# Kernel tuning notes

Measured on AMD Instinct MI355X. Metric: run time of the kernel, lower is better.

## Reference

```python
import jax, jax.numpy as jnp
import numpy as np

LOSS_WEIGHT = 1.0
EPS = 1e-08
OUT_H, OUT_W = 112, 96
NBINS = 256


def _nearest_resize(x, out_h, out_w):
    # torch F.interpolate default mode='nearest': src_idx = floor(dst_idx * in/out)
    B, C, H, W = x.shape
    hi = (jnp.arange(out_h) * H) // out_h
    wi = (jnp.arange(out_w) * W) // out_w
    return x[:, :, hi][:, :, :, wi]


def setup_inputs() -> dict:
    key = jax.random.key(0)
    k1, k2 = jax.random.split(key)
    x0 = jax.random.uniform(k1, (256, 3, 224, 192), dtype=jnp.float32) * 255.0
    img = jax.random.uniform(k2, (256, 3, OUT_H, OUT_W), dtype=jnp.float32) * 255.0
    return {"x0": x0, "img": img}


def reference(x0, img):
    # interpolate x0 to (112, 96), cast both to uint8 (truncation, values in [0,255])
    x0r = _nearest_resize(x0, OUT_H, OUT_W)
    ix = img.astype(jnp.uint8).astype(jnp.int32).ravel()   # x in hxx(img, x0)
    iy = x0r.astype(jnp.uint8).astype(jnp.int32).ravel()   # y

    # NOTE: faithful quirk — normalizer is last-dim size of img (=96), not n elements
    size = jnp.float32(img.shape[-1])

    hist_x = jnp.zeros(NBINS, jnp.float32).at[ix].add(1.0)
    hist_y = jnp.zeros(NBINS, jnp.float32).at[iy].add(1.0)
    joint = jnp.zeros(NBINS * NBINS, jnp.float32).at[ix * NBINS + iy].add(1.0)

    px = hist_x / size
    py = hist_y / size
    pxy = joint / size

    hx = -jnp.sum(px * jnp.log(px + EPS))
    hy = -jnp.sum(py * jnp.log(py + EPS))
    hxy = -jnp.sum(pxy * jnp.log(pxy + EPS))

    return LOSS_WEIGHT * (hx + hy - hxy)
```

## Files before the change

### kernel.cpp

```cpp
#include <hip/hip_runtime.h>

constexpr int NB = 256;
constexpr int OH = 112, OW = 96;
constexpr int IH = 224, IW = 192;
constexpr int NELEM = 256 * 3 * OH * OW;
constexpr int NVEC = NELEM / 4;
constexpr int JWORDS = 65536 / 4;
constexpr int NBLK = 256;


__global__ __launch_bounds__(1024) void hist_part_k(const float* __restrict__ x0,
                                                    const float* __restrict__ img,
                                                    unsigned int* __restrict__ partial) {
    __shared__ unsigned int jl[JWORDS];
    for (int w = threadIdx.x; w < JWORDS; w += 1024) jl[w] = 0u;
    __syncthreads();

    const int stride = gridDim.x * 1024;
    for (int v = blockIdx.x * 1024 + threadIdx.x; v < NVEC; v += stride) {
        const int e  = v << 2;
        const int j  = e % OW;
        const int r  = e / OW;
        const int ii = r % OH;
        const int bc = r / OH;

        const float4 im = *reinterpret_cast<const float4*>(img + e);
        const int xb = (bc * IH + 2 * ii) * IW + 2 * j;
        const float4 xa = *reinterpret_cast<const float4*>(x0 + xb);
        const float4 xc = *reinterpret_cast<const float4*>(x0 + xb + 4);

        const int b0 = ((int)im.x << 8) | (int)xa.x;
        const int b1 = ((int)im.y << 8) | (int)xa.z;
        const int b2 = ((int)im.z << 8) | (int)xc.x;
        const int b3 = ((int)im.w << 8) | (int)xc.z;
        atomicAdd(&jl[b0 >> 2], 1u << ((b0 & 3) * 8));
        atomicAdd(&jl[b1 >> 2], 1u << ((b1 & 3) * 8));
        atomicAdd(&jl[b2 >> 2], 1u << ((b2 & 3) * 8));
        atomicAdd(&jl[b3 >> 2], 1u << ((b3 & 3) * 8));
    }
    __syncthreads();
    unsigned int* __restrict__ mine = partial + (size_t)blockIdx.x * JWORDS;
    for (int w = threadIdx.x; w < JWORDS; w += 1024) mine[w] = jl[w];
}

__global__ __launch_bounds__(256) void reduce_k(const unsigned int* __restrict__ partial,
                                                unsigned int* __restrict__ joint_tot,
                                                double* __restrict__ rowent) {
    const int t = threadIdx.x;
    const int row = blockIdx.x;
    const int g = t & 15;
    const int c = t >> 4;
    const uint4* __restrict__ p4 = reinterpret_cast<const uint4*>(partial);

    uint4 s = make_uint4(0u, 0u, 0u, 0u);
    #pragma unroll
    for (int b = 0; b < 16; ++b) {
        uint4 v = p4[(size_t)(c * 16 + b) * (JWORDS / 4) + row * 16 + g];
        s.x += v.x; s.y += v.y; s.z += v.z; s.w += v.w;
    }
    __shared__ uint4 sh[256];
    sh[t] = s;
    __syncthreads();
    for (int off = 128; off >= 16; off >>= 1) {
        if (t < off) {
            uint4 a = sh[t], b2 = sh[t + off];
            a.x += b2.x; a.y += b2.y; a.z += b2.z; a.w += b2.w;
            sh[t] = a;
        }
        __syncthreads();
    }
    __shared__ unsigned int tw[64];
    if (t < 16) *reinterpret_cast<uint4*>(&tw[4 * t]) = sh[t];
    __syncthreads();

    const unsigned int cnt = (tw[t >> 2] >> ((t & 3) * 8)) & 0xFFu;
    const double inv = 1.0 / 96.0;
    const double eps = 1e-8;
    const double p = cnt * inv;
    double s2 = p * log(p + eps);
    unsigned int rs = cnt;
    for (int off = 32; off > 0; off >>= 1) {
        s2 += __shfl_down(s2, off, 64);
        rs += __shfl_down(rs, off, 64);
    }
    __shared__ double ds[4];
    __shared__ unsigned int rss[4];
    if ((t & 63) == 0) { ds[t >> 6] = s2; rss[t >> 6] = rs; }
    __syncthreads();
    if (t == 0) {
        const double sj = ds[0] + ds[1] + ds[2] + ds[3];
        const double px = (double)(rss[0] + rss[1] + rss[2] + rss[3]) * inv;
        rowent[row] = sj - px * log(px + eps);
    }
    if (t < 64) joint_tot[row * 64 + t] = tw[t];
}

__global__ __launch_bounds__(256) void final_k(const unsigned int* __restrict__ joint_tot,
                                               const double* __restrict__ rowent,
                                               float* __restrict__ out) {
    __shared__ unsigned int jl[JWORDS];
    const int t = threadIdx.x;
    {
        const uint4* __restrict__ src = reinterpret_cast<const uint4*>(joint_tot);
        uint4* __restrict__ dst = reinterpret_cast<uint4*>(jl);
        for (int i = t; i < JWORDS / 4; i += 256) dst[i] = src[i];
    }
    __syncthreads();

    const int w = t >> 2, shft = (t & 3) * 8;
    unsigned int hy = 0u;
    #pragma unroll 8
    for (int r = 0; r < 256; ++r)
        hy += (jl[r * 64 + w] >> shft) & 0xFFu;

    const double inv = 1.0 / 96.0, eps = 1e-8;
    const double py = hy * inv;
    double acc = rowent[t] - py * log(py + eps);
    for (int off = 32; off > 0; off >>= 1) acc += __shfl_down(acc, off, 64);
    __shared__ double part[4];
    if ((t & 63) == 0) part[t >> 6] = acc;
    __syncthreads();
    if (t == 0) out[0] = (float)(part[0] + part[1] + part[2] + part[3]);
}

__global__ __launch_bounds__(256) void zero_ws_k(unsigned int* __restrict__ ws) {
    int i = blockIdx.x * 256 + threadIdx.x;
    if (i < NB + NB + NB * NB) ws[i] = 0u;
}

__global__ __launch_bounds__(256) void hist_k(const float* __restrict__ x0,
                                              const float* __restrict__ img,
                                              unsigned int* __restrict__ ws) {
    __shared__ unsigned int sx[NB];
    __shared__ unsigned int sy[NB];
    if (threadIdx.x < NB) { sx[threadIdx.x] = 0u; sy[threadIdx.x] = 0u; }
    __syncthreads();
    unsigned int* __restrict__ joint = ws + 2 * NB;
    const int stride = gridDim.x * blockDim.x;
    for (int v = blockIdx.x * blockDim.x + threadIdx.x; v < NVEC; v += stride) {
        const int e  = v << 2;
        const int j  = e % OW;
        const int r  = e / OW;
        const int ii = r % OH;
        const int bc = r / OH;
        const float4 im = *reinterpret_cast<const float4*>(img + e);
        const int xb = (bc * IH + 2 * ii) * IW + 2 * j;
        const float4 xa = *reinterpret_cast<const float4*>(x0 + xb);
        const float4 xc = *reinterpret_cast<const float4*>(x0 + xb + 4);
        int ix[4] = { (int)im.x, (int)im.y, (int)im.z, (int)im.w };
        int iy[4] = { (int)xa.x, (int)xa.z, (int)xc.x, (int)xc.z };
        #pragma unroll
        for (int k = 0; k < 4; ++k) {
            atomicAdd(&sx[ix[k]], 1u);
            atomicAdd(&sy[iy[k]], 1u);
            atomicAdd(&joint[(ix[k] << 8) | iy[k]], 1u);
        }
    }
    __syncthreads();
    if (threadIdx.x < NB) {
        unsigned a = sx[threadIdx.x]; if (a) atomicAdd(ws + threadIdx.x, a);
        unsigned b = sy[threadIdx.x]; if (b) atomicAdd(ws + NB + threadIdx.x, b);
    }
}

__global__ __launch_bounds__(256) void entropy_k(const unsigned int* __restrict__ ws,
                                                 float* __restrict__ out) {
    const int t = threadIdx.x;
    const double inv = 1.0 / 96.0;
    const double eps = 1e-8;
    double acc = 0.0;
    {
        double px = ws[t] * inv;
        double py = ws[NB + t] * inv;
        acc -= px * log(px + eps);
        acc -= py * log(py + eps);
    }
    const unsigned int* __restrict__ joint = ws + 2 * NB;
    for (int k = 0; k < NB; ++k) {
        double p = joint[(t << 8) + k] * inv;
        acc += p * log(p + eps);
    }
    for (int off = 32; off > 0; off >>= 1) acc += __shfl_down(acc, off, 64);
    __shared__ double part[4];
    if ((t & 63) == 0) part[t >> 6] = acc;
    __syncthreads();
    if (t == 0) out[0] = (float)(part[0] + part[1] + part[2] + part[3]);
}

extern "C" void kernel_launch(void* const* d_in, const int* in_sizes, int n_in,
                              void* d_out, int out_size, void* d_ws, size_t ws_size,
                              hipStream_t stream) {
    const float* x0  = (const float*)d_in[0];
    const float* img = (const float*)d_in[1];
    unsigned int* ws = (unsigned int*)d_ws;
    float* out = (float*)d_out;

    const size_t J = (size_t)NBLK * JWORDS;
    const size_t need_bytes = (J + JWORDS + 512 + 64) * 4;
    if (ws_size >= need_bytes) {
        unsigned int* partial   = ws;
        unsigned int* joint_tot = ws + J;
        double*       rowent    = (double*)(ws + J + JWORDS);
        hist_part_k<<<NBLK, 1024, 0, stream>>>(x0, img, partial);
        reduce_k<<<NB, 256, 0, stream>>>(partial, joint_tot, rowent);
        final_k<<<1, 256, 0, stream>>>(joint_tot, rowent, out);
    } else {
        const int nz = NB + NB + NB * NB;
        zero_ws_k<<<(nz + 255) / 256, 256, 0, stream>>>(ws);
        hist_k<<<2048, 256, 0, stream>>>(x0, img, ws);
        entropy_k<<<1, 256, 0, stream>>>(ws, out);
    }
}
```

Measured before the change: 38.21 us.

## Unroll histogram loads by two, use nontemporal access, and drop LDS staging in final pass

```diff
diff --git a/kernel.cpp b/kernel.cpp
--- a/kernel.cpp
+++ b/kernel.cpp
@@ -8,6 +8,35 @@
 constexpr int JWORDS = 65536 / 4;
 constexpr int NBLK = 256;
 
+typedef float        f32x4 __attribute__((ext_vector_type(4)));
+typedef unsigned int u32x4 __attribute__((ext_vector_type(4)));
+
+
+__device__ __forceinline__ void load_group(const float* __restrict__ x0,
+                                           const float* __restrict__ img,
+                                           int v, f32x4& im, f32x4& xa, f32x4& xc) {
+    const int e  = v << 2;
+    const int j  = e % OW;
+    const int r  = e / OW;
+    const int ii = r % OH;
+    const int bc = r / OH;
+    im = __builtin_nontemporal_load(reinterpret_cast<const f32x4*>(img + e));
+    const int xb = (bc * IH + 2 * ii) * IW + 2 * j;
+    xa = __builtin_nontemporal_load(reinterpret_cast<const f32x4*>(x0 + xb));
+    xc = __builtin_nontemporal_load(reinterpret_cast<const f32x4*>(x0 + xb + 4));
+}
+
+__device__ __forceinline__ void scatter_group(unsigned int* __restrict__ jl,
+                                              const f32x4& im, const f32x4& xa, const f32x4& xc) {
+    const int b0 = ((int)im[0] << 8) | (int)xa[0];
+    const int b1 = ((int)im[1] << 8) | (int)xa[2];
+    const int b2 = ((int)im[2] << 8) | (int)xc[0];
+    const int b3 = ((int)im[3] << 8) | (int)xc[2];
+    atomicAdd(&jl[b0 >> 2], 1u << ((b0 & 3) * 8));
+    atomicAdd(&jl[b1 >> 2], 1u << ((b1 & 3) * 8));
+    atomicAdd(&jl[b2 >> 2], 1u << ((b2 & 3) * 8));
+    atomicAdd(&jl[b3 >> 2], 1u << ((b3 & 3) * 8));
+}
 
 __global__ __launch_bounds__(1024) void hist_part_k(const float* __restrict__ x0,
                                                     const float* __restrict__ img,
@@ -16,31 +45,24 @@
     for (int w = threadIdx.x; w < JWORDS; w += 1024) jl[w] = 0u;
     __syncthreads();
 
-    const int stride = gridDim.x * 1024;
-    for (int v = blockIdx.x * 1024 + threadIdx.x; v < NVEC; v += stride) {
-        const int e  = v << 2;
-        const int j  = e % OW;
-        const int r  = e / OW;
-        const int ii = r % OH;
-        const int bc = r / OH;
-
-        const float4 im = *reinterpret_cast<const float4*>(img + e);
-        const int xb = (bc * IH + 2 * ii) * IW + 2 * j;
-        const float4 xa = *reinterpret_cast<const float4*>(x0 + xb);
-        const float4 xc = *reinterpret_cast<const float4*>(x0 + xb + 4);
-
-        const int b0 = ((int)im.x << 8) | (int)xa.x;
-        const int b1 = ((int)im.y << 8) | (int)xa.z;
-        const int b2 = ((int)im.z << 8) | (int)xc.x;
-        const int b3 = ((int)im.w << 8) | (int)xc.z;
-        atomicAdd(&jl[b0 >> 2], 1u << ((b0 & 3) * 8));
-        atomicAdd(&jl[b1 >> 2], 1u << ((b1 & 3) * 8));
-        atomicAdd(&jl[b2 >> 2], 1u << ((b2 & 3) * 8));
-        atomicAdd(&jl[b3 >> 2], 1u << ((b3 & 3) * 8));
+    const int stride = NBLK * 1024;
+    int v = blockIdx.x * 1024 + threadIdx.x;
+    for (; v + stride < NVEC; v += 2 * stride) {
+        f32x4 im1, xa1, xc1, im2, xa2, xc2;
+        load_group(x0, img, v,          im1, xa1, xc1);
+        load_group(x0, img, v + stride, im2, xa2, xc2);
+        scatter_group(jl, im1, xa1, xc1);
+        scatter_group(jl, im2, xa2, xc2);
+    }
+    if (v < NVEC) {
+        f32x4 im1, xa1, xc1;
+        load_group(x0, img, v, im1, xa1, xc1);
+        scatter_group(jl, im1, xa1, xc1);
     }
     __syncthreads();
     unsigned int* __restrict__ mine = partial + (size_t)blockIdx.x * JWORDS;
-    for (int w = threadIdx.x; w < JWORDS; w += 1024) mine[w] = jl[w];
+    for (int w = threadIdx.x; w < JWORDS; w += 1024)
+        __builtin_nontemporal_store(jl[w], mine + w);
 }
 
 __global__ __launch_bounds__(256) void reduce_k(const unsigned int* __restrict__ partial,
@@ -50,27 +72,24 @@
     const int row = blockIdx.x;
     const int g = t & 15;
     const int c = t >> 4;
-    const uint4* __restrict__ p4 = reinterpret_cast<const uint4*>(partial);
-
-    uint4 s = make_uint4(0u, 0u, 0u, 0u);
+    const u32x4* __restrict__ p4 = reinterpret_cast<const u32x4*>(partial);
+
+    u32x4 s = {0u, 0u, 0u, 0u};
     #pragma unroll
     for (int b = 0; b < 16; ++b) {
-        uint4 v = p4[(size_t)(c * 16 + b) * (JWORDS / 4) + row * 16 + g];
-        s.x += v.x; s.y += v.y; s.z += v.z; s.w += v.w;
-    }
-    __shared__ uint4 sh[256];
+        u32x4 v = __builtin_nontemporal_load(
+            &p4[(size_t)(c * 16 + b) * (JWORDS / 4) + row * 16 + g]);
+        s += v;
+    }
+    __shared__ u32x4 sh[256];
     sh[t] = s;
     __syncthreads();
     for (int off = 128; off >= 16; off >>= 1) {
-        if (t < off) {
-            uint4 a = sh[t], b2 = sh[t + off];
-            a.x += b2.x; a.y += b2.y; a.z += b2.z; a.w += b2.w;
-            sh[t] = a;
-        }
+        if (t < off) sh[t] += sh[t + off];
         __syncthreads();
     }
     __shared__ unsigned int tw[64];
-    if (t < 16) *reinterpret_cast<uint4*>(&tw[4 * t]) = sh[t];
+    if (t < 16) *reinterpret_cast<u32x4*>(&tw[4 * t]) = sh[t];
     __syncthreads();
 
     const unsigned int cnt = (tw[t >> 2] >> ((t & 3) * 8)) & 0xFFu;
@@ -98,20 +117,23 @@
 __global__ __launch_bounds__(256) void final_k(const unsigned int* __restrict__ joint_tot,
                                                const double* __restrict__ rowent,
                                                float* __restrict__ out) {
-    __shared__ unsigned int jl[JWORDS];
     const int t = threadIdx.x;
-    {
-        const uint4* __restrict__ src = reinterpret_cast<const uint4*>(joint_tot);
-        uint4* __restrict__ dst = reinterpret_cast<uint4*>(jl);
-        for (int i = t; i < JWORDS / 4; i += 256) dst[i] = src[i];
-    }
-    __syncthreads();
-
-    const int w = t >> 2, shft = (t & 3) * 8;
-    unsigned int hy = 0u;
+    const int w = t & 63, half = t >> 6;
+    const unsigned int* __restrict__ base = joint_tot + (half * 64) * 64 + w;
+    unsigned int lo = 0u, hi = 0u;
     #pragma unroll 8
-    for (int r = 0; r < 256; ++r)
-        hy += (jl[r * 64 + w] >> shft) & 0xFFu;
+    for (int r = 0; r < 64; ++r) {
+        const unsigned int v = base[r * 64];
+        lo += v & 0x00FF00FFu;
+        hi += (v >> 8) & 0x00FF00FFu;
+    }
+    __shared__ unsigned int colp[4][256];
+    colp[half][4 * w + 0] = lo & 0xFFFFu;
+    colp[half][4 * w + 1] = hi & 0xFFFFu;
+    colp[half][4 * w + 2] = lo >> 16;
+    colp[half][4 * w + 3] = hi >> 16;
+    __syncthreads();
+    const unsigned int hy = colp[0][t] + colp[1][t] + colp[2][t] + colp[3][t];
 
     const double inv = 1.0 / 96.0, eps = 1e-8;
     const double py = hy * inv;
```

After: 33.37 us. -12.7%, faster.
